# Performance work log

Hardware: AMD Instinct MI355X
Metric: run time of the kernel (lower is better)

The kernel has to match this reference:

```python
import jax, jax.numpy as jnp
import numpy as np

B, T, D = 4, 2048, 2048
H, KV, DK = 16, 4, 128
ROPE_BASE = 10000.0


def apply_rope(x, base=ROPE_BASE):
    # x: [B, h, T, dk]; interleaved-pair rotary embedding
    dk = x.shape[-1]
    pos = jnp.arange(x.shape[2], dtype=jnp.float32)
    inv_freq = 1.0 / (base ** (jnp.arange(0, dk, 2, dtype=jnp.float32) / dk))
    ang = pos[:, None] * inv_freq[None, :]            # [T, dk/2]
    cos, sin = jnp.cos(ang), jnp.sin(ang)             # [T, dk/2]
    x1, x2 = x[..., 0::2], x[..., 1::2]               # even/odd pairs
    r1 = x1 * cos - x2 * sin
    r2 = x1 * sin + x2 * cos
    return jnp.stack([r1, r2], axis=-1).reshape(x.shape)


def setup_inputs() -> dict:
    key = jax.random.key(0)
    ks = jax.random.split(key, 5)
    s = 0.02
    return {
        "x": jax.random.normal(ks[0], (B, T, D), jnp.float32),
        "attention_mask": jnp.ones((B, T), dtype=bool),
        "Wq": jax.random.normal(ks[1], (D, D), jnp.float32) * s,
        "Wk": jax.random.normal(ks[2], (KV * DK, D), jnp.float32) * s,
        "Wv": jax.random.normal(ks[3], (KV * DK, D), jnp.float32) * s,
        "Wo": jax.random.normal(ks[4], (D, D), jnp.float32) * s,
    }


def reference(x, attention_mask, Wq, Wk, Wv, Wo):
    b, t, _ = x.shape
    # QKV projections (torch Linear: y = x @ W.T)
    Q = (x @ Wq.T).reshape(b, t, H, DK).transpose(0, 2, 1, 3)    # [B,H,T,dk]
    K = (x @ Wk.T).reshape(b, t, KV, DK).transpose(0, 2, 1, 3)   # [B,KV,T,dk]
    V = (x @ Wv.T).reshape(b, t, KV, DK).transpose(0, 2, 1, 3)
    Q = apply_rope(Q)
    K = apply_rope(K)
    # GQA: repeat kv heads
    g = H // KV
    K = jnp.repeat(K, g, axis=1)                                  # [B,H,T,dk]
    V = jnp.repeat(V, g, axis=1)
    scores = jnp.einsum("bhqd,bhkd->bhqk", Q, K) / jnp.sqrt(jnp.float32(DK))
    causal = jnp.tril(jnp.ones((t, t), dtype=bool))               # [T,T]
    mask = attention_mask[:, None, None, :] & causal[None, None]  # [B,1,T,T]
    scores = jnp.where(mask, scores, jnp.float32(-1e30))
    attn = jax.nn.softmax(scores, axis=-1)
    out = jnp.einsum("bhqk,bhkd->bhqd", attn, V)
    out = out.transpose(0, 2, 1, 3).reshape(b, t, D)
    return out @ Wo.T
```

## Files before the change

kernel.cpp:

```cpp
#include <hip/hip_runtime.h>
#include <hip/hip_bf16.h>

typedef __bf16 bf16;
typedef __attribute__((ext_vector_type(8))) __bf16 bf16x8;
typedef __attribute__((ext_vector_type(4))) float floatx4;

__device__ inline void dma16(const void* g, void* l) {
  __builtin_amdgcn_global_load_lds((const __attribute__((address_space(1))) void*)g,
                                   (__attribute__((address_space(3))) void*)l, 16, 0, 0);
}

__device__ inline void stage_tile(const bf16* gbase, size_t gs, bf16* lds,
                                  int wave, int lane) {
#pragma unroll
  for (int it = 0; it < 4; ++it) {
    int rowbase = wave * 32 + it * 8;
    const bf16* g = gbase + (size_t)(rowbase + (lane >> 3)) * gs + (lane & 7) * 8;
    dma16(g, lds + rowbase * 64);
  }
}

template <typename T> struct Raw8 {};
template <> struct Raw8<float> { float4 lo, hi; };
template <> struct Raw8<bf16>  { bf16x8 v; };
__device__ inline void raw_load(Raw8<float>& r, const float* p) {
  r.lo = *(const float4*)p; r.hi = *(const float4*)(p + 4);
}
__device__ inline void raw_load(Raw8<bf16>& r, const bf16* p) { r.v = *(const bf16x8*)p; }
__device__ inline bf16x8 cvt8(const Raw8<float>& r) {
  bf16x8 o;
  o[0] = (bf16)r.lo.x; o[1] = (bf16)r.lo.y; o[2] = (bf16)r.lo.z; o[3] = (bf16)r.lo.w;
  o[4] = (bf16)r.hi.x; o[5] = (bf16)r.hi.y; o[6] = (bf16)r.hi.z; o[7] = (bf16)r.hi.w;
  return o;
}
__device__ inline bf16x8 cvt8(const Raw8<bf16>& r) { return r.v; }

__global__ void cvt_f32_bf16(const float* __restrict__ in, bf16* __restrict__ out, int n8) {
  int i = blockIdx.x * blockDim.x + threadIdx.x;
  if (i >= n8) return;
  const float4* p = (const float4*)in + (size_t)i * 2;
  float4 a = p[0], b = p[1];
  bf16x8 o;
  o[0] = (bf16)a.x; o[1] = (bf16)a.y; o[2] = (bf16)a.z; o[3] = (bf16)a.w;
  o[4] = (bf16)b.x; o[5] = (bf16)b.y; o[6] = (bf16)b.z; o[7] = (bf16)b.w;
  *(bf16x8*)&out[(size_t)i * 8] = o;
}

#define FENCE asm volatile("" ::: "memory")
#define BAR  { FENCE; __builtin_amdgcn_s_barrier(); FENCE; }

#define MFMA_QUAD(Q)                                                        \
  __builtin_amdgcn_s_setprio(1);                                            \
  _Pragma("unroll") for (int ks = 0; ks < 2; ++ks)                          \
  _Pragma("unroll") for (int mi2 = 0; mi2 < 2; ++mi2)                       \
  _Pragma("unroll") for (int nj = 0; nj < 4; ++nj)                          \
      acc[2 * (Q) + mi2][nj] = __builtin_amdgcn_mfma_f32_16x16x32_bf16(     \
          afrag[mi2][ks], bfrag[nj][ks], acc[2 * (Q) + mi2][nj], 0, 0, 0);  \
  __builtin_amdgcn_s_setprio(0);

__device__ inline void load_bfrags(const bf16* BT, bf16x8 (&bfrag)[4][2],
                                   int wn, int lrow, int quad, int cswz) {
#pragma unroll
  for (int nj = 0; nj < 4; ++nj)
#pragma unroll
    for (int ks = 0; ks < 2; ++ks)
      bfrag[nj][ks] = *(const bf16x8*)&BT[(wn * 64 + nj * 16 + lrow) * 64 +
                                          ((ks * 32 + quad * 8) ^ cswz)];
}
__device__ inline void load_afrags(const bf16* AT, bf16x8 (&afrag)[2][2], int q,
                                   int wm, int lrow, int quad, int cswz) {
#pragma unroll
  for (int mi2 = 0; mi2 < 2; ++mi2)
#pragma unroll
    for (int ks = 0; ks < 2; ++ks)
      afrag[mi2][ks] = *(const bf16x8*)&AT[(wm * 128 + (2 * q + mi2) * 16 + lrow) * 64 +
                                           ((ks * 32 + quad * 8) ^ cswz)];
}

template <bool QKV>
__global__ __launch_bounds__(512, 2) void gemm256(
    const bf16* __restrict__ A, const bf16* __restrict__ Bw,
    bf16* __restrict__ Qb, bf16* __restrict__ Kb, bf16* __restrict__ Vb,
    float* __restrict__ Cf, int NBN) {
  extern __shared__ __align__(16) bf16 lds[];
  bf16* As0 = lds;
  bf16* Bs0 = lds + 16384;
  bf16* As1 = lds + 32768;
  bf16* Bs1 = lds + 49152;

  const int t = threadIdx.x;
  const int wave = t >> 6, lane = t & 63;
  const int lrow = lane & 15, quad = lane >> 4;
  const int wm = wave >> 2, wn = wave & 3;
  const int cswz = ((lrow >> 2) & 1) << 4;

  const int nwg = gridDim.x * gridDim.y;
  int bid = blockIdx.y * gridDim.x + blockIdx.x;
  const int cpx = nwg >> 3;
  int swz = (bid & 7) * cpx + (bid >> 3);
  const int bm = swz / NBN, bn = swz % NBN;

  const int K = 2048;
  const bf16* Ab = A + (size_t)bm * 256 * K;
  const bf16* Bb = Bw + (size_t)bn * 256 * K;

  const int str = wave * 8 + (lane >> 3);
  const int stc = (((lane & 7) ^ (((lane >> 5) & 1) << 1)) * 8);
  auto stA = [&](bf16* dst, int tt, int h) {
    const bf16* g = Ab + (size_t)(h * 128) * K + tt * 64;
    bf16* l = dst + h * 8192;
#pragma unroll
    for (int it = 0; it < 2; ++it)
      dma16(g + (size_t)(it * 64 + str) * K + stc, l + (it * 64 + wave * 8) * 64);
  };
  auto stB = [&](bf16* dst, int tt, int h) {
    const bf16* g = Bb + (size_t)(h * 128) * K + tt * 64;
    bf16* l = dst + h * 8192;
#pragma unroll
    for (int it = 0; it < 2; ++it)
      dma16(g + (size_t)(it * 64 + str) * K + stc, l + (it * 64 + wave * 8) * 64);
  };

  floatx4 acc[8][4] = {};
  bf16x8 bfrag[4][2], afrag[2][2];

  stA(As0, 0, 0); stA(As0, 0, 1);
  stB(Bs0, 0, 0); stB(Bs0, 0, 1);
  stB(Bs1, 1, 0); stB(Bs1, 1, 1);
  asm volatile("s_waitcnt vmcnt(4)" ::: "memory");
  BAR;

#pragma unroll 1
  for (int g = 0; g < 15; ++g) {
    const int a = 2 * g;
    load_bfrags(Bs0, bfrag, wn, lrow, quad, cswz);
    load_afrags(As0, afrag, 0, wm, lrow, quad, cswz);
    stA(As1, a + 1, 0);
    BAR; MFMA_QUAD(0); BAR;
    load_afrags(As0, afrag, 1, wm, lrow, quad, cswz);
    stA(As1, a + 1, 1);
    BAR; MFMA_QUAD(1); BAR;
    load_afrags(As0, afrag, 2, wm, lrow, quad, cswz);
    stB(Bs0, a + 2, 0);
    BAR; MFMA_QUAD(2); BAR;
    load_afrags(As0, afrag, 3, wm, lrow, quad, cswz);
    stB(Bs0, a + 2, 1);
    asm volatile("s_waitcnt vmcnt(4)" ::: "memory");
    BAR; MFMA_QUAD(3); BAR;
    load_bfrags(Bs1, bfrag, wn, lrow, quad, cswz);
    load_afrags(As1, afrag, 0, wm, lrow, quad, cswz);
    stA(As0, a + 2, 0);
    BAR; MFMA_QUAD(0); BAR;
    load_afrags(As1, afrag, 1, wm, lrow, quad, cswz);
    stA(As0, a + 2, 1);
    BAR; MFMA_QUAD(1); BAR;
    load_afrags(As1, afrag, 2, wm, lrow, quad, cswz);
    stB(Bs1, a + 3, 0);
    BAR; MFMA_QUAD(2); BAR;
    load_afrags(As1, afrag, 3, wm, lrow, quad, cswz);
    stB(Bs1, a + 3, 1);
    asm volatile("s_waitcnt vmcnt(4)" ::: "memory");
    BAR; MFMA_QUAD(3); BAR;
  }
  {
    load_bfrags(Bs0, bfrag, wn, lrow, quad, cswz);
    load_afrags(As0, afrag, 0, wm, lrow, quad, cswz);
    stA(As1, 31, 0);
    BAR; MFMA_QUAD(0); BAR;
    load_afrags(As0, afrag, 1, wm, lrow, quad, cswz);
    stA(As1, 31, 1);
    BAR; MFMA_QUAD(1); BAR;
    load_afrags(As0, afrag, 2, wm, lrow, quad, cswz);
    BAR; MFMA_QUAD(2); BAR;
    load_afrags(As0, afrag, 3, wm, lrow, quad, cswz);
    asm volatile("s_waitcnt vmcnt(0)" ::: "memory");
    BAR; MFMA_QUAD(3); BAR;
    load_bfrags(Bs1, bfrag, wn, lrow, quad, cswz);
    load_afrags(As1, afrag, 0, wm, lrow, quad, cswz);
    BAR; MFMA_QUAD(0); BAR;
    load_afrags(As1, afrag, 1, wm, lrow, quad, cswz);
    BAR; MFMA_QUAD(1); BAR;
    load_afrags(As1, afrag, 2, wm, lrow, quad, cswz);
    BAR; MFMA_QUAD(2); BAR;
    load_afrags(As1, afrag, 3, wm, lrow, quad, cswz);
    BAR; MFMA_QUAD(3); BAR;
  }

  if constexpr (QKV) {
    bf16* Cp; int ld, n0;
    const int gn = bn * 256;
    if (gn < 2048)      { Cp = Qb; ld = 2048; n0 = gn; }
    else if (gn < 2560) { Cp = Kb; ld = 512;  n0 = gn - 2048; }
    else                { Cp = Vb; ld = 512;  n0 = gn - 2560; }
#pragma unroll
    for (int mi = 0; mi < 8; ++mi)
#pragma unroll
      for (int nj = 0; nj < 4; ++nj)
#pragma unroll
        for (int r = 0; r < 4; ++r) {
          int m = bm * 256 + wm * 128 + mi * 16 + quad * 4 + r;
          int n = n0 + wn * 64 + nj * 16 + lrow;
          Cp[(size_t)m * ld + n] = (bf16)acc[mi][nj][r];
        }
  } else {
#pragma unroll
    for (int mi = 0; mi < 8; ++mi)
#pragma unroll
      for (int nj = 0; nj < 4; ++nj)
#pragma unroll
        for (int r = 0; r < 4; ++r) {
          int m = bm * 256 + wm * 128 + mi * 16 + quad * 4 + r;
          int n = bn * 256 + wn * 64 + nj * 16 + lrow;
          Cf[(size_t)m * 2048 + n] = acc[mi][nj][r];
        }
  }
}

template <typename TB>
__global__ __launch_bounds__(256) void gemm_a16(
    const bf16* __restrict__ A, const TB* __restrict__ B,
    float* __restrict__ C, int M, int N, int K) {
  __shared__ __align__(16) bf16 As[128 * 64];
  __shared__ __align__(16) bf16 Bs[128 * 64];
  const int t = threadIdx.x;
  const int wave = t >> 6, lane = t & 63;
  const int lrow = lane & 15, quad = lane >> 4;
  const int wm = (wave >> 1) * 64, wn = (wave & 1) * 64;
  const int bm = blockIdx.y, bn = blockIdx.x;

  const bf16* Ab = A + (size_t)bm * 128 * K;
  const TB* Bb = B + (size_t)bn * 128 * K;

  constexpr bool B_ASYNC = __is_same(TB, bf16);
  const int row_ = t >> 3, cc_ = (t & 7) * 8;
  Raw8<TB> bR[4];
  auto loadB = [&](int k0) {
#pragma unroll
    for (int it = 0; it < 4; ++it)
      raw_load(bR[it], &Bb[(size_t)(row_ + it * 32) * K + k0 + cc_]);
  };
  if constexpr (!B_ASYNC) loadB(0);

  floatx4 acc[4][4] = {};

  for (int k0 = 0; k0 < K; k0 += 64) {
    __syncthreads();
    stage_tile(Ab + k0, K, As, wave, lane);
    if constexpr (B_ASYNC) {
      stage_tile((const bf16*)Bb + k0, K, Bs, wave, lane);
    } else {
#pragma unroll
      for (int it = 0; it < 4; ++it)
        *(bf16x8*)&Bs[(row_ + it * 32) * 64 + cc_] = cvt8(bR[it]);
      if (k0 + 64 < K) loadB(k0 + 64);
    }
    __syncthreads();
#pragma unroll
    for (int ks = 0; ks < 2; ++ks) {
      bf16x8 af[4], bfr[4];
#pragma unroll
      for (int i = 0; i < 4; ++i)
        af[i] = *(const bf16x8*)&As[(wm + i * 16 + lrow) * 64 + ks * 32 + quad * 8];
#pragma unroll
      for (int j = 0; j < 4; ++j)
        bfr[j] = *(const bf16x8*)&Bs[(wn + j * 16 + lrow) * 64 + ks * 32 + quad * 8];
#pragma unroll
      for (int i = 0; i < 4; ++i)
#pragma unroll
        for (int j = 0; j < 4; ++j)
          acc[i][j] = __builtin_amdgcn_mfma_f32_16x16x32_bf16(af[i], bfr[j], acc[i][j], 0, 0, 0);
    }
  }
#pragma unroll
  for (int i = 0; i < 4; ++i)
#pragma unroll
    for (int j = 0; j < 4; ++j)
#pragma unroll
      for (int r = 0; r < 4; ++r) {
        int m = bm * 128 + wm + i * 16 + quad * 4 + r;
        int n = bn * 128 + wn + j * 16 + lrow;
        C[(size_t)m * N + n] = acc[i][j][r];
      }
}

__global__ void rope_kernel(bf16* __restrict__ buf, int lg, int nchunks) {
  int idx = blockIdx.x * blockDim.x + threadIdx.x;
  if (idx >= nchunks) return;
  int row = idx >> (lg - 3);
  int off = (idx - (row << (lg - 3))) * 8;
  int d = off & 127;
  int pos = row & 2047;
  bf16x8 v = *(const bf16x8*)&buf[((size_t)row << lg) + off];
  bf16x8 o;
#pragma unroll
  for (int p = 0; p < 4; ++p) {
    int i = (d >> 1) + p;
    float inv = __expf(-(float)i * 0.14391156683f);
    float ang = (float)pos * inv;
    float sv = sinf(ang), cv = cosf(ang);
    float x1 = (float)v[2 * p], x2 = (float)v[2 * p + 1];
    o[2 * p]     = (bf16)(x1 * cv - x2 * sv);
    o[2 * p + 1] = (bf16)(x1 * sv + x2 * cv);
  }
  *(bf16x8*)&buf[((size_t)row << lg) + off] = o;
}

#define K_LD 136
#define V_LD 72
#define P_LD 72
#define SC2 0.12751879623162f
#define M2  17.312340490667f

__global__ __launch_bounds__(256) void attn_kernel(
    bf16* __restrict__ Qb, const bf16* __restrict__ Kb,
    const bf16* __restrict__ Vb) {
  __shared__ __align__(16) bf16 SKP[128 * P_LD];
  __shared__ __align__(16) bf16 Vt[128 * V_LD];
  bf16* Ks = SKP;
  bf16* Ps = SKP;

  const int t = threadIdx.x;
  const int wave = t >> 6, lane = t & 63;
  const int lrow = lane & 15, quad = lane >> 4;
  const int bh = blockIdx.x;
  const int b = bh >> 4, h = bh & 15;
  const int qt = 15 - blockIdx.y;
  const int kvh = h >> 2;
  const int wq = wave * 32;
  const size_t qrow0 = (size_t)b * 2048 + (size_t)qt * 128;
  const size_t krowb = (size_t)b * 2048;

  bf16x8 qf[2][4];
#pragma unroll
  for (int ti = 0; ti < 2; ++ti)
#pragma unroll
    for (int ks = 0; ks < 4; ++ks)
      qf[ti][ks] = *(const bf16x8*)&Qb[(qrow0 + wq + ti * 16 + lrow) * 2048 +
                                       h * 128 + ks * 32 + quad * 8];

  bf16x8 ones;
#pragma unroll
  for (int j = 0; j < 8; ++j) ones[j] = (bf16)1.0f;

  floatx4 o_acc[2][8] = {};
  floatx4 l_acc[2] = {};

  const int nkt = (qt + 1) * 2;

  const int kkey_ = t >> 4, kdc_ = (t & 15) * 8;
  const int vdc_ = t >> 6, vk_ = t & 63;

  bf16x8 kreg[4], vreg[4];
  auto loadKV = [&](int kt) {
    const size_t krow0 = krowb + (size_t)kt * 64;
#pragma unroll
    for (int it = 0; it < 4; ++it) {
      kreg[it] = *(const bf16x8*)&Kb[(krow0 + kkey_ + it * 16) * 512 + kvh * 128 + kdc_];
      vreg[it] = *(const bf16x8*)&Vb[(krow0 + vk_) * 512 + kvh * 128 + (vdc_ + it * 4) * 8];
    }
  };
  loadKV(0);

  for (int kt = 0; kt < nkt; ++kt) {
    __syncthreads();
#pragma unroll
    for (int it = 0; it < 4; ++it) {
      *(bf16x8*)&Ks[(kkey_ + it * 16) * K_LD + kdc_] = kreg[it];
      int dc = (vdc_ + it * 4) * 8;
#pragma unroll
      for (int j = 0; j < 8; ++j) Vt[(dc + j) * V_LD + vk_] = vreg[it][j];
    }
    if (kt + 1 < nkt) loadKV(kt + 1);
    __syncthreads();

    floatx4 s_acc[2][4] = {};
    __builtin_amdgcn_s_setprio(1);
#pragma unroll
    for (int ks = 0; ks < 4; ++ks) {
      bf16x8 kf[4];
#pragma unroll
      for (int tj = 0; tj < 4; ++tj)
        kf[tj] = *(const bf16x8*)&Ks[(tj * 16 + lrow) * K_LD + ks * 32 + quad * 8];
#pragma unroll
      for (int ti = 0; ti < 2; ++ti)
#pragma unroll
        for (int tj = 0; tj < 4; ++tj)
          s_acc[ti][tj] = __builtin_amdgcn_mfma_f32_16x16x32_bf16(
              qf[ti][ks], kf[tj], s_acc[ti][tj], 0, 0, 0);
    }
    __builtin_amdgcn_s_setprio(0);

    __syncthreads();

    const bool diag = (kt * 64 + 63) > (qt * 128 + wq);
#pragma unroll
    for (int ti = 0; ti < 2; ++ti)
#pragma unroll
      for (int tj = 0; tj < 4; ++tj)
#pragma unroll
        for (int r = 0; r < 4; ++r) {
          float p = exp2f(fmaf(s_acc[ti][tj][r], SC2, -M2));
          if (diag) {
            int qrow = qt * 128 + wq + ti * 16 + quad * 4 + r;
            int kcol = kt * 64 + tj * 16 + lrow;
            p = (kcol > qrow) ? 0.f : p;
          }
          Ps[(wq + ti * 16 + quad * 4 + r) * P_LD + tj * 16 + lrow] = (bf16)p;
        }

    __builtin_amdgcn_s_setprio(1);
#pragma unroll
    for (int ks2 = 0; ks2 < 2; ++ks2) {
      bf16x8 pf[2];
#pragma unroll
      for (int ti = 0; ti < 2; ++ti) {
        pf[ti] = *(const bf16x8*)&Ps[(wq + ti * 16 + lrow) * P_LD + ks2 * 32 + quad * 8];
        l_acc[ti] = __builtin_amdgcn_mfma_f32_16x16x32_bf16(pf[ti], ones, l_acc[ti], 0, 0, 0);
      }
#pragma unroll
      for (int tjo = 0; tjo < 8; ++tjo) {
        bf16x8 vf = *(const bf16x8*)&Vt[(tjo * 16 + lrow) * V_LD + ks2 * 32 + quad * 8];
#pragma unroll
        for (int ti = 0; ti < 2; ++ti)
          o_acc[ti][tjo] = __builtin_amdgcn_mfma_f32_16x16x32_bf16(
              pf[ti], vf, o_acc[ti][tjo], 0, 0, 0);
      }
    }
    __builtin_amdgcn_s_setprio(0);
  }

#pragma unroll
  for (int ti = 0; ti < 2; ++ti)
#pragma unroll
    for (int r = 0; r < 4; ++r) {
      float invl = 1.f / l_acc[ti][r];
#pragma unroll
      for (int tjo = 0; tjo < 8; ++tjo) {
        int m = wq + ti * 16 + quad * 4 + r;
        int n = h * 128 + tjo * 16 + lrow;
        Qb[(qrow0 + m) * 2048 + n] = (bf16)(o_acc[ti][tjo][r] * invl);
      }
    }
}

extern "C" void kernel_launch(void* const* d_in, const int* in_sizes, int n_in,
                              void* d_out, int out_size, void* d_ws, size_t ws_size,
                              hipStream_t stream) {
  const float* x  = (const float*)d_in[0];
  const float* Wq = (const float*)d_in[2];
  const float* Wk = (const float*)d_in[3];
  const float* Wv = (const float*)d_in[4];
  const float* Wo = (const float*)d_in[5];
  float* out = (float*)d_out;

  const int Mrows = 8192;
  const size_t qElems = (size_t)Mrows * 2048;
  const size_t kvElems = (size_t)Mrows * 512;

  bf16* Kb  = (bf16*)d_out;
  bf16* Vb  = Kb + kvElems;
  bf16* xb  = Vb + kvElems;
  bf16* Wqkvb = xb + qElems;
  bf16* Wqb = Wqkvb;
  bf16* Wkb = Wqb + (size_t)2048 * 2048;
  bf16* Wvb = Wkb + (size_t)512 * 2048;

  bf16* Qb  = (bf16*)d_ws;
  bf16* Wob = Qb + qElems;
  const bool woBf16 = ws_size >= (qElems + (size_t)2048 * 2048) * sizeof(bf16);

  static bool s_attr = false;
  if (!s_attr) {
    (void)hipFuncSetAttribute((const void*)&gemm256<true>,
                              hipFuncAttributeMaxDynamicSharedMemorySize, 131072);
    (void)hipFuncSetAttribute((const void*)&gemm256<false>,
                              hipFuncAttributeMaxDynamicSharedMemorySize, 131072);
    s_attr = true;
  }

  dim3 blk(256);
  cvt_f32_bf16<<<dim3(8192), blk, 0, stream>>>(x, xb, (int)(qElems / 8));
  cvt_f32_bf16<<<dim3(2048), blk, 0, stream>>>(Wq, Wqb, 2048 * 2048 / 8);
  cvt_f32_bf16<<<dim3(512),  blk, 0, stream>>>(Wk, Wkb, 512 * 2048 / 8);
  cvt_f32_bf16<<<dim3(512),  blk, 0, stream>>>(Wv, Wvb, 512 * 2048 / 8);
  if (woBf16)
    cvt_f32_bf16<<<dim3(2048), blk, 0, stream>>>(Wo, Wob, 2048 * 2048 / 8);

  gemm256<true><<<dim3(12, 32), dim3(512), 131072, stream>>>(
      xb, Wqkvb, Qb, Kb, Vb, nullptr, 12);

  rope_kernel<<<dim3((int)(qElems / 8 + 255) / 256), blk, 0, stream>>>(Qb, 11, (int)(qElems / 8));
  rope_kernel<<<dim3((int)(kvElems / 8 + 255) / 256), blk, 0, stream>>>(Kb, 9, (int)(kvElems / 8));

  attn_kernel<<<dim3(64, 16), blk, 0, stream>>>(Qb, Kb, Vb);

  if (woBf16)
    gemm256<false><<<dim3(8, 32), dim3(512), 131072, stream>>>(
        Qb, Wob, nullptr, nullptr, nullptr, out, 8);
  else
    gemm_a16<float><<<dim3(16, 64), blk, 0, stream>>>(Qb, Wo, out, Mrows, 2048, 2048);
}
```

Before: 480.8 us.

## Split attention query tile across eight waves of sixteen rows each

The attention kernel now launches 512 threads per block. Each of the eight waves owns 16 query rows instead of each of four waves owning 32. The per-wave accumulators, Q fragments and K/V staging registers are halved, and the K/V global loads are spread over twice as many threads. The aim is more waves in flight for latency hiding and lower register pressure. The cost is that every wave now reads the full K and V tiles from LDS for fewer rows, which doubles LDS read traffic per query row and halves MFMA reuse of each K/V fragment.

```diff
diff --git a/kernel.cpp b/kernel.cpp
--- a/kernel.cpp
+++ b/kernel.cpp
@@ -311,7 +311,7 @@
 #define SC2 0.12751879623162f
 #define M2  17.312340490667f
 
-__global__ __launch_bounds__(256) void attn_kernel(
+__global__ __launch_bounds__(512) void attn_kernel(
     bf16* __restrict__ Qb, const bf16* __restrict__ Kb,
     const bf16* __restrict__ Vb) {
   __shared__ __align__(16) bf16 SKP[128 * P_LD];
@@ -326,37 +326,35 @@
   const int b = bh >> 4, h = bh & 15;
   const int qt = 15 - blockIdx.y;
   const int kvh = h >> 2;
-  const int wq = wave * 32;
+  const int wq = wave * 16;
   const size_t qrow0 = (size_t)b * 2048 + (size_t)qt * 128;
   const size_t krowb = (size_t)b * 2048;
 
-  bf16x8 qf[2][4];
-#pragma unroll
-  for (int ti = 0; ti < 2; ++ti)
-#pragma unroll
-    for (int ks = 0; ks < 4; ++ks)
-      qf[ti][ks] = *(const bf16x8*)&Qb[(qrow0 + wq + ti * 16 + lrow) * 2048 +
-                                       h * 128 + ks * 32 + quad * 8];
+  bf16x8 qf[4];
+#pragma unroll
+  for (int ks = 0; ks < 4; ++ks)
+    qf[ks] = *(const bf16x8*)&Qb[(qrow0 + wq + lrow) * 2048 +
+                                 h * 128 + ks * 32 + quad * 8];
 
   bf16x8 ones;
 #pragma unroll
   for (int j = 0; j < 8; ++j) ones[j] = (bf16)1.0f;
 
-  floatx4 o_acc[2][8] = {};
-  floatx4 l_acc[2] = {};
+  floatx4 o_acc[8] = {};
+  floatx4 l_acc = {};
 
   const int nkt = (qt + 1) * 2;
 
   const int kkey_ = t >> 4, kdc_ = (t & 15) * 8;
   const int vdc_ = t >> 6, vk_ = t & 63;
 
-  bf16x8 kreg[4], vreg[4];
+  bf16x8 kreg[2], vreg[2];
   auto loadKV = [&](int kt) {
     const size_t krow0 = krowb + (size_t)kt * 64;
 #pragma unroll
-    for (int it = 0; it < 4; ++it) {
-      kreg[it] = *(const bf16x8*)&Kb[(krow0 + kkey_ + it * 16) * 512 + kvh * 128 + kdc_];
-      vreg[it] = *(const bf16x8*)&Vb[(krow0 + vk_) * 512 + kvh * 128 + (vdc_ + it * 4) * 8];
+    for (int it = 0; it < 2; ++it) {
+      kreg[it] = *(const bf16x8*)&Kb[(krow0 + kkey_ + it * 32) * 512 + kvh * 128 + kdc_];
+      vreg[it] = *(const bf16x8*)&Vb[(krow0 + vk_) * 512 + kvh * 128 + (vdc_ + it * 8) * 8];
     }
   };
   loadKV(0);
@@ -364,16 +362,16 @@
   for (int kt = 0; kt < nkt; ++kt) {
     __syncthreads();
 #pragma unroll
-    for (int it = 0; it < 4; ++it) {
-      *(bf16x8*)&Ks[(kkey_ + it * 16) * K_LD + kdc_] = kreg[it];
-      int dc = (vdc_ + it * 4) * 8;
+    for (int it = 0; it < 2; ++it) {
+      *(bf16x8*)&Ks[(kkey_ + it * 32) * K_LD + kdc_] = kreg[it];
+      int dc = (vdc_ + it * 8) * 8;
 #pragma unroll
       for (int j = 0; j < 8; ++j) Vt[(dc + j) * V_LD + vk_] = vreg[it][j];
     }
     if (kt + 1 < nkt) loadKV(kt + 1);
     __syncthreads();
 
-    floatx4 s_acc[2][4] = {};
+    floatx4 s_acc[4] = {};
     __builtin_amdgcn_s_setprio(1);
 #pragma unroll
     for (int ks = 0; ks < 4; ++ks) {
@@ -382,11 +380,9 @@
       for (int tj = 0; tj < 4; ++tj)
         kf[tj] = *(const bf16x8*)&Ks[(tj * 16 + lrow) * K_LD + ks * 32 + quad * 8];
 #pragma unroll
-      for (int ti = 0; ti < 2; ++ti)
-#pragma unroll
-        for (int tj = 0; tj < 4; ++tj)
-          s_acc[ti][tj] = __builtin_amdgcn_mfma_f32_16x16x32_bf16(
-              qf[ti][ks], kf[tj], s_acc[ti][tj], 0, 0, 0);
+      for (int tj = 0; tj < 4; ++tj)
+        s_acc[tj] = __builtin_amdgcn_mfma_f32_16x16x32_bf16(
+            qf[ks], kf[tj], s_acc[tj], 0, 0, 0);
     }
     __builtin_amdgcn_s_setprio(0);
 
@@ -394,53 +390,43 @@
 
     const bool diag = (kt * 64 + 63) > (qt * 128 + wq);
 #pragma unroll
-    for (int ti = 0; ti < 2; ++ti)
-#pragma unroll
-      for (int tj = 0; tj < 4; ++tj)
-#pragma unroll
-        for (int r = 0; r < 4; ++r) {
-          float p = exp2f(fmaf(s_acc[ti][tj][r], SC2, -M2));
-          if (diag) {
-            int qrow = qt * 128 + wq + ti * 16 + quad * 4 + r;
-            int kcol = kt * 64 + tj * 16 + lrow;
-            p = (kcol > qrow) ? 0.f : p;
-          }
-          Ps[(wq + ti * 16 + quad * 4 + r) * P_LD + tj * 16 + lrow] = (bf16)p;
+    for (int tj = 0; tj < 4; ++tj)
+#pragma unroll
+      for (int r = 0; r < 4; ++r) {
+        float p = exp2f(fmaf(s_acc[tj][r], SC2, -M2));
+        if (diag) {
+          int qrow = qt * 128 + wq + quad * 4 + r;
+          int kcol = kt * 64 + tj * 16 + lrow;
+          p = (kcol > qrow) ? 0.f : p;
         }
+        Ps[(wq + quad * 4 + r) * P_LD + tj * 16 + lrow] = (bf16)p;
+      }
 
     __builtin_amdgcn_s_setprio(1);
 #pragma unroll
     for (int ks2 = 0; ks2 < 2; ++ks2) {
-      bf16x8 pf[2];
-#pragma unroll
-      for (int ti = 0; ti < 2; ++ti) {
-        pf[ti] = *(const bf16x8*)&Ps[(wq + ti * 16 + lrow) * P_LD + ks2 * 32 + quad * 8];
-        l_acc[ti] = __builtin_amdgcn_mfma_f32_16x16x32_bf16(pf[ti], ones, l_acc[ti], 0, 0, 0);
-      }
+      bf16x8 pf = *(const bf16x8*)&Ps[(wq + lrow) * P_LD + ks2 * 32 + quad * 8];
+      l_acc = __builtin_amdgcn_mfma_f32_16x16x32_bf16(pf, ones, l_acc, 0, 0, 0);
 #pragma unroll
       for (int tjo = 0; tjo < 8; ++tjo) {
         bf16x8 vf = *(const bf16x8*)&Vt[(tjo * 16 + lrow) * V_LD + ks2 * 32 + quad * 8];
-#pragma unroll
-        for (int ti = 0; ti < 2; ++ti)
-          o_acc[ti][tjo] = __builtin_amdgcn_mfma_f32_16x16x32_bf16(
-              pf[ti], vf, o_acc[ti][tjo], 0, 0, 0);
+        o_acc[tjo] = __builtin_amdgcn_mfma_f32_16x16x32_bf16(
+            pf, vf, o_acc[tjo], 0, 0, 0);
       }
     }
     __builtin_amdgcn_s_setprio(0);
   }
 
 #pragma unroll
-  for (int ti = 0; ti < 2; ++ti)
-#pragma unroll
-    for (int r = 0; r < 4; ++r) {
-      float invl = 1.f / l_acc[ti][r];
-#pragma unroll
-      for (int tjo = 0; tjo < 8; ++tjo) {
-        int m = wq + ti * 16 + quad * 4 + r;
-        int n = h * 128 + tjo * 16 + lrow;
-        Qb[(qrow0 + m) * 2048 + n] = (bf16)(o_acc[ti][tjo][r] * invl);
-      }
-    }
+  for (int r = 0; r < 4; ++r) {
+    float invl = 1.f / l_acc[r];
+#pragma unroll
+    for (int tjo = 0; tjo < 8; ++tjo) {
+      int m = wq + quad * 4 + r;
+      int n = h * 128 + tjo * 16 + lrow;
+      Qb[(qrow0 + m) * 2048 + n] = (bf16)(o_acc[tjo][r] * invl);
+    }
+  }
 }
 
 extern "C" void kernel_launch(void* const* d_in, const int* in_sizes, int n_in,
@@ -492,7 +478,7 @@
   rope_kernel<<<dim3((int)(qElems / 8 + 255) / 256), blk, 0, stream>>>(Qb, 11, (int)(qElems / 8));
   rope_kernel<<<dim3((int)(kvElems / 8 + 255) / 256), blk, 0, stream>>>(Kb, 9, (int)(kvElems / 8));
 
-  attn_kernel<<<dim3(64, 16), blk, 0, stream>>>(Qb, Kb, Vb);
+  attn_kernel<<<dim3(64, 16), dim3(512), 0, stream>>>(Qb, Kb, Vb);
 
   if (woBf16)
     gemm256<false><<<dim3(8, 32), dim3(512), 131072, stream>>>(
```

New measurement: 474.0 us. No clear change (-1.4%).

## Fuse conversion kernels, move Q RoPE into attention, split K/P shared buffers

Applied to the files above, without the earlier changes.

Merges the five fp32-to-bf16 conversion launches into one kernel that dispatches by index range. Q RoPE is now applied in registers after the attention kernel loads Q, which removes a full read and write pass over Q; the old rope_kernel now runs only on K. Ks and Ps get separate shared buffers, which lets one __syncthreads per key tile be dropped at the cost of more LDS per block. The fast __expf/__sinf/__cosf intrinsics may lose accuracy at large angles.

```diff
diff --git a/kernel.cpp b/kernel.cpp
--- a/kernel.cpp
+++ b/kernel.cpp
@@ -35,15 +35,26 @@
 }
 __device__ inline bf16x8 cvt8(const Raw8<bf16>& r) { return r.v; }
 
-__global__ void cvt_f32_bf16(const float* __restrict__ in, bf16* __restrict__ out, int n8) {
+__global__ void cvt_all(const float* __restrict__ x,  const float* __restrict__ Wq,
+                        const float* __restrict__ Wk, const float* __restrict__ Wv,
+                        const float* __restrict__ Wo,
+                        bf16* __restrict__ xb,  bf16* __restrict__ Wqb,
+                        bf16* __restrict__ Wkb, bf16* __restrict__ Wvb,
+                        bf16* __restrict__ Wob, int nWo) {
   int i = blockIdx.x * blockDim.x + threadIdx.x;
-  if (i >= n8) return;
-  const float4* p = (const float4*)in + (size_t)i * 2;
+  const float* src; bf16* dst; int off;
+  if (i < 2097152)                      { src = x;  dst = xb;  off = i; }
+  else if (i < 2097152 + 524288)        { src = Wq; dst = Wqb; off = i - 2097152; }
+  else if (i < 2097152 + 655360)        { src = Wk; dst = Wkb; off = i - (2097152 + 524288); }
+  else if (i < 2097152 + 786432)        { src = Wv; dst = Wvb; off = i - (2097152 + 655360); }
+  else if (i < 2097152 + 786432 + nWo)  { src = Wo; dst = Wob; off = i - (2097152 + 786432); }
+  else return;
+  const float4* p = (const float4*)src + (size_t)off * 2;
   float4 a = p[0], b = p[1];
   bf16x8 o;
   o[0] = (bf16)a.x; o[1] = (bf16)a.y; o[2] = (bf16)a.z; o[3] = (bf16)a.w;
   o[4] = (bf16)b.x; o[5] = (bf16)b.y; o[6] = (bf16)b.z; o[7] = (bf16)b.w;
-  *(bf16x8*)&out[(size_t)i * 8] = o;
+  *(bf16x8*)&dst[(size_t)off * 8] = o;
 }
 
 #define FENCE asm volatile("" ::: "memory")
@@ -314,10 +325,9 @@
 __global__ __launch_bounds__(256) void attn_kernel(
     bf16* __restrict__ Qb, const bf16* __restrict__ Kb,
     const bf16* __restrict__ Vb) {
-  __shared__ __align__(16) bf16 SKP[128 * P_LD];
+  __shared__ __align__(16) bf16 Ks[64 * K_LD];
   __shared__ __align__(16) bf16 Vt[128 * V_LD];
-  bf16* Ks = SKP;
-  bf16* Ps = SKP;
+  __shared__ __align__(16) bf16 Ps[128 * P_LD];
 
   const int t = threadIdx.x;
   const int wave = t >> 6, lane = t & 63;
@@ -338,6 +348,23 @@
       qf[ti][ks] = *(const bf16x8*)&Qb[(qrow0 + wq + ti * 16 + lrow) * 2048 +
                                        h * 128 + ks * 32 + quad * 8];
 
+#pragma unroll
+  for (int ti = 0; ti < 2; ++ti) {
+    float pos = (float)(qt * 128 + wq + ti * 16 + lrow);
+#pragma unroll
+    for (int ks = 0; ks < 4; ++ks)
+#pragma unroll
+      for (int p = 0; p < 4; ++p) {
+        int i = ks * 16 + quad * 4 + p;
+        float inv = __expf(-(float)i * 0.14391156683f);
+        float ang = pos * inv;
+        float sv = __sinf(ang), cv = __cosf(ang);
+        float x1 = (float)qf[ti][ks][2 * p], x2 = (float)qf[ti][ks][2 * p + 1];
+        qf[ti][ks][2 * p]     = (bf16)(x1 * cv - x2 * sv);
+        qf[ti][ks][2 * p + 1] = (bf16)(x1 * sv + x2 * cv);
+      }
+  }
+
   bf16x8 ones;
 #pragma unroll
   for (int j = 0; j < 8; ++j) ones[j] = (bf16)1.0f;
@@ -389,8 +416,6 @@
               qf[ti][ks], kf[tj], s_acc[ti][tj], 0, 0, 0);
     }
     __builtin_amdgcn_s_setprio(0);
-
-    __syncthreads();
 
     const bool diag = (kt * 64 + 63) > (qt * 128 + wq);
 #pragma unroll
@@ -478,25 +503,22 @@
     s_attr = true;
   }
 
-  dim3 blk(256);
-  cvt_f32_bf16<<<dim3(8192), blk, 0, stream>>>(x, xb, (int)(qElems / 8));
-  cvt_f32_bf16<<<dim3(2048), blk, 0, stream>>>(Wq, Wqb, 2048 * 2048 / 8);
-  cvt_f32_bf16<<<dim3(512),  blk, 0, stream>>>(Wk, Wkb, 512 * 2048 / 8);
-  cvt_f32_bf16<<<dim3(512),  blk, 0, stream>>>(Wv, Wvb, 512 * 2048 / 8);
-  if (woBf16)
-    cvt_f32_bf16<<<dim3(2048), blk, 0, stream>>>(Wo, Wob, 2048 * 2048 / 8);
+  const int nWo = woBf16 ? 524288 : 0;
+  const int totalChunks = 2097152 + 786432 + nWo;
+  cvt_all<<<dim3(totalChunks / 256), dim3(256), 0, stream>>>(
+      x, Wq, Wk, Wv, Wo, xb, Wqb, Wkb, Wvb, Wob, nWo);
 
   gemm256<true><<<dim3(12, 32), dim3(512), 131072, stream>>>(
       xb, Wqkvb, Qb, Kb, Vb, nullptr, 12);
 
-  rope_kernel<<<dim3((int)(qElems / 8 + 255) / 256), blk, 0, stream>>>(Qb, 11, (int)(qElems / 8));
-  rope_kernel<<<dim3((int)(kvElems / 8 + 255) / 256), blk, 0, stream>>>(Kb, 9, (int)(kvElems / 8));
-
-  attn_kernel<<<dim3(64, 16), blk, 0, stream>>>(Qb, Kb, Vb);
+  rope_kernel<<<dim3((int)(kvElems / 8 + 255) / 256), dim3(256), 0, stream>>>(
+      Kb, 9, (int)(kvElems / 8));
+
+  attn_kernel<<<dim3(64, 16), dim3(256), 0, stream>>>(Qb, Kb, Vb);
 
   if (woBf16)
     gemm256<false><<<dim3(8, 32), dim3(512), 131072, stream>>>(
         Qb, Wob, nullptr, nullptr, nullptr, out, 8);
   else
-    gemm_a16<float><<<dim3(16, 64), blk, 0, stream>>>(Qb, Wo, out, Mrows, 2048, 2048);
-}
+    gemm_a16<float><<<dim3(16, 64), dim3(256), 0, stream>>>(Qb, Wo, out, Mrows, 2048, 2048);
+}
```

Result: faster. 459.7 us (-4.4%).
